# Kernel tuning notes

Hardware: AMD Instinct MI355X
Metric: run time of the kernel (lower is better)

## Reference

```python
import math
import jax, jax.numpy as jnp
import numpy as np
from jax import lax

D = 384; NHEAD = 12; NLAYERS = 4; H = 128; WIN = (128, 24); NS = (1, 10); B = 256; CONV_C = 128

def _interleave(s, c):
    # [s0,c0,s1,c1,...] along last dim (matches 0::2=sin, 1::2=cos)
    return jnp.stack([s, c], axis=-1).reshape(s.shape[:-1] + (s.shape[-1] * 2,))

def _pos_encoding():
    d3 = D // 3
    div = jnp.exp(jnp.arange(0, d3, 2, dtype=jnp.float32) * (-math.log(10000.0) / d3))
    coord = jnp.arange(H, dtype=jnp.float32) - H // 2
    pe1d = _interleave(jnp.sin(coord[:, None] * div), jnp.cos(coord[:, None] * div))  # (H, d3)
    pe_y = jnp.broadcast_to(pe1d[:, None, :], (H, H, d3))
    pe_x = jnp.broadcast_to(pe1d[None, :, :], (H, H, d3))
    ws = jnp.array(WIN, dtype=jnp.float32)
    pe_w = _interleave(jnp.sin(ws[:, None] * div), jnp.cos(ws[:, None] * div))  # (2, d3)
    pe_yx = jnp.concatenate([pe_y, pe_x], axis=-1)  # (H, H, 2*d3)
    pe = jnp.concatenate([
        jnp.broadcast_to(pe_yx[:, :, None, :], (H, H, len(WIN), 2 * d3)),
        jnp.broadcast_to(pe_w[None, None, :, :], (H, H, len(WIN), d3))], axis=-1)
    return pe  # (H, H, 2, D)

def _windows(img3, pos, ws):
    # img3: (B,3,H,W); pos: (n,2) int. Crop [y1:y2, x1:x2] then zero-pad bottom/right to ws x ws.
    hw = ws // 2
    y = jnp.clip(pos[:, 0], 0, H - 1); x = jnp.clip(pos[:, 1], 0, H - 1)
    y1 = jnp.maximum(0, y - hw); y2 = jnp.minimum(H, y + hw)
    x1 = jnp.maximum(0, x - hw); x2 = jnp.minimum(H, x + hw)
    r = jnp.arange(ws)
    rows = y1[:, None] + r; cols = x1[:, None] + r  # (n, ws)
    mask = (rows < y2[:, None])[:, :, None] & (cols < x2[:, None])[:, None, :]  # (n, ws, ws)
    win = img3[:, :, jnp.clip(rows, 0, H - 1)[:, :, None], jnp.clip(cols, 0, H - 1)[:, None, :]]  # (B,3,n,ws,ws)
    win = jnp.where(mask[None, None], win, 0.0)
    return jnp.transpose(win, (0, 2, 1, 3, 4))  # (B, n, 3, ws, ws)

def _layer_norm(x, g, b):
    m = x.mean(-1, keepdims=True)
    v = ((x - m) ** 2).mean(-1, keepdims=True)
    return (x - m) / jnp.sqrt(v + 1e-5) * g + b

def _encoder_layer(x, Wqkv, bqkv, Wo, bo, g1, b1, g2, b2, W1, bf1, W2, bf2):
    Bsz, S, _ = x.shape
    dh = D // NHEAD
    qkv = x @ Wqkv.T + bqkv
    q, k, v = jnp.split(qkv, 3, axis=-1)
    heads = lambda t: t.reshape(Bsz, S, NHEAD, dh).transpose(0, 2, 1, 3)
    q, k, v = heads(q), heads(k), heads(v)
    att = jax.nn.softmax(jnp.einsum('bhqd,bhkd->bhqk', q, k) / math.sqrt(dh), axis=-1)
    o = jnp.einsum('bhqk,bhkd->bhqd', att, v).transpose(0, 2, 1, 3).reshape(Bsz, S, D)
    x = _layer_norm(x + o @ Wo.T + bo, g1, b1)
    ff = jax.nn.relu(x @ W1.T + bf1) @ W2.T + bf2
    return _layer_norm(x + ff, g2, b2)

def _normalize(v):
    return v / jnp.maximum(jnp.linalg.norm(v, axis=1, keepdims=True), 1e-12)

def _forward(pos0, pos1, rgb_image, conv_w, conv_b, ext_w, ext_b, proj_w, proj_b,
             Wqkv, bqkv, Wo, bo, ln1g, ln1b, ln2g, ln2b, Wff1, bff1, Wff2, bff2,
             rw1, rb1, rw2, rb2, uw1, ub1, uw2, ub2):
    Bsz = rgb_image.shape[0]
    img3 = rgb_image[:, :3]
    win0 = _windows(img3, pos0, WIN[0]).reshape(Bsz * NS[0], 3, WIN[0], WIN[0])
    win1 = _windows(img3, pos1, WIN[1])  # (B, 10, 3, 24, 24)
    h = lax.conv_general_dilated(win0, conv_w, (4, 4), 'SAME')
    h = jax.nn.relu(h + conv_b[None, :, None, None])
    f0 = (h.mean((2, 3)) @ ext_w.T + ext_b).reshape(Bsz, NS[0], D)
    f1 = win1.reshape(Bsz, NS[1], -1) @ proj_w.T + proj_b  # (B,10,D)
    feats = jnp.concatenate([f0, f1], axis=1)  # (B, 11, D)
    pe = _pos_encoding()
    pp = jnp.concatenate([
        jnp.concatenate([pos0, jnp.zeros((NS[0], 1), pos0.dtype)], axis=1),
        jnp.concatenate([pos1, jnp.ones((NS[1], 1), pos1.dtype)], axis=1)], axis=0)  # (11, 3)
    pf = pe[pp[:, 0], pp[:, 1], pp[:, 2]]  # (11, D)
    x = feats + pf[None]
    for i in range(NLAYERS):
        x = _encoder_layer(x, Wqkv[i], bqkv[i], Wo[i], bo[i], ln1g[i], ln1b[i],
                           ln2g[i], ln2b[i], Wff1[i], bff1[i], Wff2[i], bff2[i])
    m = x.mean(axis=1)
    r = jax.nn.relu(m @ rw1.T + rb1) @ rw2.T + rb2
    r1, r2 = r[:, :3], r[:, 3:]
    r2 = r2 - jnp.sum(r1 * r2, axis=1, keepdims=True) * r1
    r3 = jnp.cross(r1, r2)
    R = jnp.concatenate([_normalize(r1), _normalize(r2), _normalize(r3)], axis=1)
    uv = jax.nn.sigmoid(jax.nn.relu(m @ uw1.T + ub1) @ uw2.T + ub2)
    return (uv, R)

def setup_inputs():
    key = jax.random.key(0)
    ks = iter(jax.random.split(key, 40))
    w = lambda *s: jax.random.normal(next(ks), s, jnp.float32) * 0.02
    return dict(
        rgb_image=jax.random.uniform(next(ks), (B, 4, H, H), jnp.float32),
        pos0=jax.random.randint(next(ks), (NS[0], 2), 0, H).astype(jnp.int32),
        pos1=jax.random.randint(next(ks), (NS[1], 2), 0, H).astype(jnp.int32),
        conv_w=w(CONV_C, 3, 7, 7), conv_b=jnp.zeros((CONV_C,), jnp.float32),
        ext_w=w(D, CONV_C), ext_b=jnp.zeros((D,), jnp.float32),
        proj_w=w(D, WIN[1] * WIN[1] * 3), proj_b=jnp.zeros((D,), jnp.float32),
        Wqkv=w(NLAYERS, 3 * D, D), bqkv=jnp.zeros((NLAYERS, 3 * D), jnp.float32),
        Wo=w(NLAYERS, D, D), bo=jnp.zeros((NLAYERS, D), jnp.float32),
        ln1g=jnp.ones((NLAYERS, D), jnp.float32), ln1b=jnp.zeros((NLAYERS, D), jnp.float32),
        ln2g=jnp.ones((NLAYERS, D), jnp.float32), ln2b=jnp.zeros((NLAYERS, D), jnp.float32),
        Wff1=w(NLAYERS, 2048, D), bff1=jnp.zeros((NLAYERS, 2048), jnp.float32),
        Wff2=w(NLAYERS, D, 2048), bff2=jnp.zeros((NLAYERS, D), jnp.float32),
        rw1=w(D, D), rb1=jnp.zeros((D,), jnp.float32),
        rw2=w(6, D), rb2=jnp.zeros((6,), jnp.float32),
        uw1=w(D, D), ub1=jnp.zeros((D,), jnp.float32),
        uw2=w(2, D), ub2=jnp.zeros((2,), jnp.float32),
    )

def reference(rgb_image, pos0, pos1, conv_w, conv_b, ext_w, ext_b, proj_w, proj_b,
              Wqkv, bqkv, Wo, bo, ln1g, ln1b, ln2g, ln2b, Wff1, bff1, Wff2, bff2,
              rw1, rb1, rw2, rb2, uw1, ub1, uw2, ub2):
    return _forward(pos0, pos1, rgb_image, conv_w, conv_b, ext_w, ext_b, proj_w, proj_b,
                    Wqkv, bqkv, Wo, bo, ln1g, ln1b, ln2g, ln2b, Wff1, bff1, Wff2, bff2,
                    rw1, rb1, rw2, rb2, uw1, ub1, uw2, ub2)
```

## Files before the change

kernel.cpp:

```cpp
#include <hip/hip_runtime.h>
#include <hip/hip_bf16.h>

#define B_ 256
#define S_ 11
#define D_ 384
#define NHEAD_ 12

typedef const float* bfp;
typedef __attribute__((ext_vector_type(8))) __bf16 bf16x8;
typedef __attribute__((ext_vector_type(4))) float f32x4;

__device__ __forceinline__ bf16x8 ld8_b64(const __bf16* p) {
    union { unsigned long long q[2]; bf16x8 v; } u;
    u.q[0] = *reinterpret_cast<const unsigned long long*>(p);
    u.q[1] = *reinterpret_cast<const unsigned long long*>(p + 4);
    return u.v;
}

__device__ __forceinline__ void gl16(const __bf16* g, __bf16* l) {
    __builtin_amdgcn_global_load_lds(
        (const __attribute__((address_space(1))) void*)g,
        (__attribute__((address_space(3))) void*)l, 16, 0, 0);
}

__global__ void prep_k(const float* __restrict__ proj_w, const float* __restrict__ Wqkv,
                       const float* __restrict__ Wo, const float* __restrict__ Wff1,
                       const float* __restrict__ Wff2,
                       __bf16* __restrict__ projWb, __bf16* __restrict__ WqkvB,
                       __bf16* __restrict__ WoB, __bf16* __restrict__ Wff1B,
                       __bf16* __restrict__ Wff2B,
                       const float* __restrict__ cw, __bf16* __restrict__ wpad,
                       const int* __restrict__ pos0, const int* __restrict__ pos1,
                       float* __restrict__ pf)
{
    int i = blockIdx.x * 256 + threadIdx.x;
    const float* s; __bf16* d; int off;
    if      (i < 165888)  { s = proj_w; d = projWb; off = i; }
    else if (i < 608256)  { s = Wqkv;   d = WqkvB;  off = i - 165888; }
    else if (i < 755712)  { s = Wo;     d = WoB;    off = i - 608256; }
    else if (i < 1542144) { s = Wff1;   d = Wff1B;  off = i - 755712; }
    else if (i < 2328576) { s = Wff2;   d = Wff2B;  off = i - 1542144; }
    else if (i < 2331648) {
        int e = i - 2328576;
        int r = e >> 5, g = e & 31;
        if (g >= 24) return;
        union { __bf16 h[8]; uint4 u; } w;
        #pragma unroll
        for (int kx = 0; kx < 8; ++kx) {
            float v = 0.f;
            if (g < 21 && kx < 7) v = cw[(size_t)r * 147 + g * 7 + kx];
            w.h[kx] = (__bf16)v;
        }
        *reinterpret_cast<uint4*>(&wpad[(size_t)r * 192 + g * 8]) = w.u;
        return;
    }
    else if (i < 2332032) {
        int dd0 = i - 2331648;
        const float c1 = -logf(10000.f) / 128.f;
        for (int ss = 0; ss < 11; ++ss) {
            int py, px, pw;
            if (ss == 0) { py = pos0[0]; px = pos0[1]; pw = 0; }
            else { py = pos1[(ss - 1) * 2]; px = pos1[(ss - 1) * 2 + 1]; pw = 1; }
            float coordv; int dd = dd0;
            if (dd0 < 128) coordv = (float)(py - 64);
            else if (dd0 < 256) { coordv = (float)(px - 64); dd = dd0 - 128; }
            else { coordv = (pw == 0) ? 128.f : 24.f; dd = dd0 - 256; }
            int ii = dd >> 1;
            float div = expf((float)(2 * ii) * c1);
            float ang = coordv * div;
            pf[ss * 384 + dd0] = (dd & 1) ? cosf(ang) : sinf(ang);
        }
        return;
    }
    else return;
    float4 v = reinterpret_cast<const float4*>(s)[off];
    union { __bf16 h[4]; unsigned long long u; } p;
    p.h[0] = (__bf16)v.x; p.h[1] = (__bf16)v.y;
    p.h[2] = (__bf16)v.z; p.h[3] = (__bf16)v.w;
    reinterpret_cast<unsigned long long*>(d)[off] = p.u;
}

__global__ __launch_bounds__(256) void gemm_bb_k(
    const __bf16* __restrict__ A, const __bf16* __restrict__ W,
    const float* __restrict__ bias, const float* __restrict__ resid,
    void* __restrict__ C_, int M, int N, int K, int mode, int outBf16, int kChunk)
{
    __shared__ __align__(16) __bf16 AsF[2][4096];
    __shared__ __align__(16) __bf16 WsF[2][4096];
    const int tid = threadIdx.x;
    const int bm = blockIdx.y * 64, bn = blockIdx.x * 64;
    const int z = blockIdx.z;
    int kStart = 0, kEnd = K;
    if (kChunk) { kStart = z * kChunk; kEnd = min(K, kStart + kChunk); }
    const int lane = tid & 63, wv = tid >> 6;
    const int wr = (wv >> 1) * 32, wc = (wv & 1) * 32;
    const int lr = lane & 15, lk = lane >> 4;
    const int c1 = tid + 256;
    const int r0 = tid >> 3, j0 = (tid & 7) ^ (r0 & 7);
    const int r1 = c1 >> 3,  j1 = (c1 & 7) ^ (r1 & 7);
    const size_t gaoff0 = (size_t)(bm + r0) * K + j0 * 8;
    const size_t gaoff1 = (size_t)(bm + r1) * K + j1 * 8;
    const size_t gwoff0 = (size_t)(bn + r0) * K + j0 * 8;
    const size_t gwoff1 = (size_t)(bn + r1) * K + j1 * 8;
    f32x4 acc[2][2] = {};

#define STAGE_(bf, kk) do {                                   \
        gl16(A + gaoff0 + (kk), &AsF[bf][(wv << 9)]);         \
        gl16(A + gaoff1 + (kk), &AsF[bf][2048 + (wv << 9)]);  \
        gl16(W + gwoff0 + (kk), &WsF[bf][(wv << 9)]);         \
        gl16(W + gwoff1 + (kk), &WsF[bf][2048 + (wv << 9)]);  \
    } while (0)

    STAGE_(0, kStart);
    __syncthreads();
    int cur = 0;
    for (int k0 = kStart; k0 < kEnd; k0 += 64) {
        if (k0 + 64 < kEnd) STAGE_(cur ^ 1, k0 + 64);
        const __bf16* Ab = AsF[cur];
        const __bf16* Wb = WsF[cur];
        #pragma unroll
        for (int s = 0; s < 2; ++s) {
            int j = s * 4 + lk;
            int ra0 = wr + lr,  ra1 = wr + 16 + lr;
            int rw0 = wc + lr,  rw1 = wc + 16 + lr;
            bf16x8 a0 = *reinterpret_cast<const bf16x8*>(&Ab[ra0 * 64 + ((j ^ (ra0 & 7)) << 3)]);
            bf16x8 a1 = *reinterpret_cast<const bf16x8*>(&Ab[ra1 * 64 + ((j ^ (ra1 & 7)) << 3)]);
            bf16x8 w0 = *reinterpret_cast<const bf16x8*>(&Wb[rw0 * 64 + ((j ^ (rw0 & 7)) << 3)]);
            bf16x8 w1 = *reinterpret_cast<const bf16x8*>(&Wb[rw1 * 64 + ((j ^ (rw1 & 7)) << 3)]);
            acc[0][0] = __builtin_amdgcn_mfma_f32_16x16x32_bf16(a0, w0, acc[0][0], 0, 0, 0);
            acc[0][1] = __builtin_amdgcn_mfma_f32_16x16x32_bf16(a0, w1, acc[0][1], 0, 0, 0);
            acc[1][0] = __builtin_amdgcn_mfma_f32_16x16x32_bf16(a1, w0, acc[1][0], 0, 0, 0);
            acc[1][1] = __builtin_amdgcn_mfma_f32_16x16x32_bf16(a1, w1, acc[1][1], 0, 0, 0);
        }
        __syncthreads();
        cur ^= 1;
    }
#undef STAGE_
    if (kChunk) {
        float* Cp = (float*)C_ + (size_t)z * M * N;
        #pragma unroll
        for (int m = 0; m < 2; ++m)
            #pragma unroll
            for (int n = 0; n < 2; ++n) {
                int col = bn + wc + n * 16 + lr;
                #pragma unroll
                for (int i = 0; i < 4; ++i) {
                    int row = bm + wr + m * 16 + lk * 4 + i;
                    Cp[(size_t)row * N + col] = acc[m][n][i];
                }
            }
    } else {
        #pragma unroll
        for (int m = 0; m < 2; ++m)
            #pragma unroll
            for (int n = 0; n < 2; ++n) {
                int col = bn + wc + n * 16 + lr;
                float bcol = bias[col];
                #pragma unroll
                for (int i = 0; i < 4; ++i) {
                    int row = bm + wr + m * 16 + lk * 4 + i;
                    float v = acc[m][n][i] + bcol;
                    if (mode == 1) v = fmaxf(v, 0.f);
                    if (mode == 2) v += resid[(size_t)row * N + col];
                    if (outBf16) ((__bf16*)C_)[(size_t)row * N + col] = (__bf16)v;
                    else         ((float*)C_)[(size_t)row * N + col] = v;
                }
            }
    }
}

__global__ __launch_bounds__(256) void convgemm_k(
    bfp __restrict__ img, const __bf16* __restrict__ wpad, bfp __restrict__ cb,
    const int* __restrict__ pos0, float* __restrict__ f0pre)
{
    __shared__ __align__(16) __bf16 Wlds[64][200];
    __shared__ __align__(16) __bf16 P[3][12][136];
    const int tid = threadIdx.x;
    const int blk = blockIdx.x;
    const int b = blk >> 3;
    const int bn = ((blk >> 2) & 1) * 64;
    const int mtg = blk & 3;
    int y = min(max(pos0[0], 0), 127), x = min(max(pos0[1], 0), 127);
    int y1 = max(0, y - 64), y2 = min(128, y + 64);
    int x1 = max(0, x - 64), x2 = min(128, x + 64);
    const int lane = tid & 63, wv = tid >> 6;
    const int wr = (wv >> 1) * 32, wc = (wv & 1) * 32;
    const int lr = lane & 15, lk = lane >> 4;
    const int oyl = wr >> 5;
    const int ox0 = lr, ox1 = 16 + lr;

    for (int e = tid; e < 1536; e += 256) {
        int r = e / 24, g = e - r * 24;
        uint4 q = *reinterpret_cast<const uint4*>(&wpad[(size_t)(bn + r) * 192 + g * 8]);
        *reinterpret_cast<uint4*>(&Wlds[r][g * 8]) = q;
    }

    float s0 = 0.f, s1 = 0.f;
    const float bc0 = cb[bn + wc + lr];
    const float bc1 = cb[bn + wc + 16 + lr];

    for (int t = 0; t < 4; ++t) {
        int mt = mtg * 4 + t;
        __syncthreads();
        for (int e = tid; e < 2448; e += 256) {
            int c = e / 816, rem = e - c * 816;
            int r2 = rem / 68, ip2 = (rem - r2 * 68) * 2;
            int rl = mt * 8 - 1 + r2;
            bool rok = (rl >= 0) && ((y1 + rl) < y2);
            const float* row = img + ((size_t)(b * 4 + c) * 128 + y1 + rl) * 128 + x1;
            int cl0 = ip2 - 1, cl1 = ip2;
            float v0 = 0.f, v1 = 0.f;
            if (rok && cl0 >= 0 && (x1 + cl0) < x2) v0 = row[cl0];
            if (rok && (x1 + cl1) < x2)             v1 = row[cl1];
            union { __bf16 h[2]; unsigned int u; } p;
            p.h[0] = (__bf16)v0; p.h[1] = (__bf16)v1;
            *reinterpret_cast<unsigned int*>(&P[c][r2][ip2]) = p.u;
        }
        __syncthreads();
        f32x4 acc[2][2] = {};
        #pragma unroll
        for (int kk = 0; kk < 6; ++kk) {
            int g = kk * 4 + lk;
            int c = g / 7, ky = g - c * 7;
            if (g >= 21) { c = 0; ky = 0; }
            const __bf16* prow = &P[c][oyl * 4 + ky][0];
            bf16x8 a0 = ld8_b64(prow + ox0 * 4);
            bf16x8 a1 = ld8_b64(prow + ox1 * 4);
            bf16x8 w0 = *reinterpret_cast<const bf16x8*>(&Wlds[wc + lr][g * 8]);
            bf16x8 w1 = *reinterpret_cast<const bf16x8*>(&Wlds[wc + 16 + lr][g * 8]);
            acc[0][0] = __builtin_amdgcn_mfma_f32_16x16x32_bf16(a0, w0, acc[0][0], 0, 0, 0);
            acc[0][1] = __builtin_amdgcn_mfma_f32_16x16x32_bf16(a0, w1, acc[0][1], 0, 0, 0);
            acc[1][0] = __builtin_amdgcn_mfma_f32_16x16x32_bf16(a1, w0, acc[1][0], 0, 0, 0);
            acc[1][1] = __builtin_amdgcn_mfma_f32_16x16x32_bf16(a1, w1, acc[1][1], 0, 0, 0);
        }
        #pragma unroll
        for (int m = 0; m < 2; ++m)
            #pragma unroll
            for (int i = 0; i < 4; ++i) {
                s0 += fmaxf(acc[m][0][i] + bc0, 0.f);
                s1 += fmaxf(acc[m][1][i] + bc1, 0.f);
            }
    }
    s0 += __shfl_xor(s0, 16); s0 += __shfl_xor(s0, 32);
    s1 += __shfl_xor(s1, 16); s1 += __shfl_xor(s1, 32);
    if (lk == 0) {
        atomicAdd(&f0pre[b * 128 + bn + wc + lr],      s0 * (1.f / 1024.f));
        atomicAdd(&f0pre[b * 128 + bn + wc + 16 + lr], s1 * (1.f / 1024.f));
    }
}

#define BM 64
#define BN 64
#define BK 16
__global__ __launch_bounds__(256) void gemm_k(
    const float* __restrict__ A, bfp __restrict__ W,
    bfp __restrict__ bias, const float* __restrict__ resid,
    float* __restrict__ C, int M, int N, int K, int mode)
{
    __shared__ __align__(16) float As[BK][BM + 4];
    __shared__ __align__(16) float Ws[BK][BN + 4];
    const int tx = threadIdx.x & 15, ty = threadIdx.x >> 4;
    const int bm = blockIdx.y * BM, bn = blockIdx.x * BN;
    float acc[4][4] = {};
    for (int k0 = 0; k0 < K; k0 += BK) {
        for (int e = threadIdx.x; e < BM * BK; e += 256) {
            int r = e >> 4, kk = e & 15;
            As[kk][r] = A[(size_t)(bm + r) * K + k0 + kk];
        }
        for (int e = threadIdx.x; e < BN * BK; e += 256) {
            int c = e >> 4, kk = e & 15;
            Ws[kk][c] = W[(size_t)(bn + c) * K + k0 + kk];
        }
        __syncthreads();
        #pragma unroll
        for (int kk = 0; kk < BK; ++kk) {
            float4 av = *reinterpret_cast<const float4*>(&As[kk][ty * 4]);
            float4 wv = *reinterpret_cast<const float4*>(&Ws[kk][tx * 4]);
            float a[4] = {av.x, av.y, av.z, av.w};
            float w[4] = {wv.x, wv.y, wv.z, wv.w};
            #pragma unroll
            for (int i = 0; i < 4; ++i)
                #pragma unroll
                for (int j = 0; j < 4; ++j) acc[i][j] += a[i] * w[j];
        }
        __syncthreads();
    }
    #pragma unroll
    for (int i = 0; i < 4; ++i) {
        int row = bm + ty * 4 + i;
        #pragma unroll
        for (int j = 0; j < 4; ++j) {
            int col = bn + tx * 4 + j;
            float v = acc[i][j] + bias[col];
            if (mode == 1) v = fmaxf(v, 0.f);
            if (mode == 2) v += resid[(size_t)row * N + col];
            C[(size_t)row * N + col] = v;
        }
    }
}

__global__ void f0_k(const float* __restrict__ f0pre, bfp __restrict__ ew,
                     bfp __restrict__ eb, float* __restrict__ fbuf0)
{
    int b = blockIdx.x, d = threadIdx.x;
    __shared__ float pre[128];
    if (d < 128) pre[d] = f0pre[b * 128 + d];
    __syncthreads();
    float acc = eb[d];
    for (int co = 0; co < 128; ++co) acc += pre[co] * ew[d * 128 + co];
    fbuf0[b * 384 + d] = acc;
}

__global__ void win1_k(bfp __restrict__ img, const int* __restrict__ pos1,
                       __bf16* __restrict__ w1)
{
    int i = blockIdx.x * 256 + threadIdx.x;
    if (i >= B_ * 10 * 1728) return;
    int cc = i % 24, r = (i / 24) % 24, c = (i / 576) % 3, s = (i / 1728) % 10, b = i / 17280;
    int y = min(max(pos1[s * 2], 0), 127), x = min(max(pos1[s * 2 + 1], 0), 127);
    int y1 = max(0, y - 12), y2 = min(128, y + 12);
    int x1 = max(0, x - 12), x2 = min(128, x + 12);
    float v = 0.f;
    if ((y1 + r) < y2 && (x1 + cc) < x2)
        v = img[((size_t)(b * 4 + c) * 128 + (y1 + r)) * 128 + (x1 + cc)];
    w1[i] = (__bf16)v;
}

__global__ void assemble_k(const float* __restrict__ f0, const float* __restrict__ p0,
                           const float* __restrict__ p1, const float* __restrict__ projb,
                           const float* __restrict__ pf, float* __restrict__ x,
                           __bf16* __restrict__ xb)
{
    int i = blockIdx.x * 256 + threadIdx.x;
    if (i >= B_ * S_ * D_) return;
    int d = i % 384, s = (i / 384) % 11, b = i / (384 * 11);
    float f;
    if (s == 0) f = f0[b * 384 + d];
    else {
        size_t o = ((size_t)(b * 10) + (s - 1)) * 384 + d;
        f = p0[o] + p1[o] + projb[d];
    }
    float v = f + pf[s * 384 + d];
    x[i] = v;
    xb[i] = (__bf16)v;
}

__global__ __launch_bounds__(128) void attn_k(const float* __restrict__ qkv,
                                              __bf16* __restrict__ obuf)
{
    int b = blockIdx.x / NHEAD_, h = blockIdx.x % NHEAD_;
    __shared__ float q[11][32], k[11][32], v[11][32], att[11][12];
    for (int e = threadIdx.x; e < 352; e += 128) {
        int s = e >> 5, d = e & 31;
        size_t base = (size_t)(b * 11 + s) * 1152 + h * 32 + d;
        q[s][d] = qkv[base];
        k[s][d] = qkv[base + 384];
        v[s][d] = qkv[base + 768];
    }
    __syncthreads();
    if (threadIdx.x < 121) {
        int i = threadIdx.x / 11, j = threadIdx.x % 11;
        float s = 0.f;
        #pragma unroll
        for (int d = 0; d < 32; ++d) s += q[i][d] * k[j][d];
        att[i][j] = s * 0.17677669529663687f;
    }
    __syncthreads();
    if (threadIdx.x < 11) {
        int i = threadIdx.x;
        float mx = att[i][0];
        for (int j = 1; j < 11; ++j) mx = fmaxf(mx, att[i][j]);
        float e_[11], sum = 0.f;
        for (int j = 0; j < 11; ++j) { e_[j] = expf(att[i][j] - mx); sum += e_[j]; }
        float inv = 1.f / sum;
        for (int j = 0; j < 11; ++j) att[i][j] = e_[j] * inv;
    }
    __syncthreads();
    for (int e = threadIdx.x; e < 352; e += 128) {
        int i = e >> 5, d = e & 31;
        float s = 0.f;
        #pragma unroll
        for (int j = 0; j < 11; ++j) s += att[i][j] * v[j][d];
        obuf[(size_t)(b * 11 + i) * 384 + h * 32 + d] = (__bf16)s;
    }
}

__global__ __launch_bounds__(512) void ln_k(const float* __restrict__ parts, int nparts,
                                            const float* __restrict__ resid,
                                            const float* __restrict__ bias,
                                            bfp g, bfp be, float* __restrict__ xo,
                                            __bf16* __restrict__ xb)
{
    int row = blockIdx.x * 8 + (threadIdx.x >> 6);
    int lane = threadIdx.x & 63;
    const size_t MN = (size_t)2816 * 384;
    float v[6];
    float s = 0.f, sq = 0.f;
    #pragma unroll
    for (int j = 0; j < 6; ++j) {
        int d = lane + 64 * j;
        size_t off = (size_t)row * 384 + d;
        float t = resid[off] + bias[d];
        for (int z = 0; z < nparts; ++z) t += parts[z * MN + off];
        v[j] = t; s += t; sq += t * t;
    }
    #pragma unroll
    for (int o = 32; o >= 1; o >>= 1) { s += __shfl_xor(s, o); sq += __shfl_xor(sq, o); }
    float mean = s * (1.f / 384.f);
    float var = sq * (1.f / 384.f) - mean * mean;
    float inv = rsqrtf(var + 1e-5f);
    float* xr = xo + (size_t)row * 384;
    __bf16* xbr = xb + (size_t)row * 384;
    #pragma unroll
    for (int j = 0; j < 6; ++j) {
        int d = lane + 64 * j;
        float o = (v[j] - mean) * inv * g[d] + be[d];
        xr[d] = o;
        xbr[d] = (__bf16)o;
    }
}

__global__ void mean_k(const float* __restrict__ x, float* __restrict__ m)
{
    int b = blockIdx.x, d = threadIdx.x;
    float s = 0.f;
    for (int si = 0; si < 11; ++si) s += x[((size_t)b * 11 + si) * 384 + d];
    m[b * 384 + d] = s * (1.f / 11.f);
}

__global__ __launch_bounds__(64) void head_k(const float* __restrict__ h1,
    const float* __restrict__ h2, bfp __restrict__ rw2, bfp __restrict__ rb2,
    bfp __restrict__ uw2, bfp __restrict__ ub2, float* __restrict__ out)
{
    int b = blockIdx.x, lane = threadIdx.x;
    float acc[8] = {};
    for (int d = lane; d < 384; d += 64) {
        float a1 = h1[b * 384 + d], a2 = h2[b * 384 + d];
        #pragma unroll
        for (int o = 0; o < 6; ++o) acc[o] += a1 * rw2[o * 384 + d];
        acc[6] += a2 * uw2[d];
        acc[7] += a2 * uw2[384 + d];
    }
    #pragma unroll
    for (int o = 0; o < 8; ++o)
        #pragma unroll
        for (int off = 32; off >= 1; off >>= 1) acc[o] += __shfl_xor(acc[o], off);
    if (lane == 0) {
        float r[6];
        for (int o = 0; o < 6; ++o) r[o] = acc[o] + rb2[o];
        float u0 = acc[6] + ub2[0], u1 = acc[7] + ub2[1];
        float dot12 = r[0] * r[3] + r[1] * r[4] + r[2] * r[5];
        float q2x = r[3] - dot12 * r[0], q2y = r[4] - dot12 * r[1], q2z = r[5] - dot12 * r[2];
        float q3x = r[1] * q2z - r[2] * q2y;
        float q3y = r[2] * q2x - r[0] * q2z;
        float q3z = r[0] * q2y - r[1] * q2x;
        float n1 = fmaxf(sqrtf(r[0]*r[0] + r[1]*r[1] + r[2]*r[2]), 1e-12f);
        float n2 = fmaxf(sqrtf(q2x*q2x + q2y*q2y + q2z*q2z), 1e-12f);
        float n3 = fmaxf(sqrtf(q3x*q3x + q3y*q3y + q3z*q3z), 1e-12f);
        out[b * 2 + 0] = 1.f / (1.f + expf(-u0));
        out[b * 2 + 1] = 1.f / (1.f + expf(-u1));
        float* R = out + B_ * 2 + b * 9;
        R[0] = r[0] / n1; R[1] = r[1] / n1; R[2] = r[2] / n1;
        R[3] = q2x / n2;  R[4] = q2y / n2;  R[5] = q2z / n2;
        R[6] = q3x / n3;  R[7] = q3y / n3;  R[8] = q3z / n3;
    }
}

extern "C" void kernel_launch(void* const* d_in, const int* in_sizes, int n_in,
                              void* d_out, int out_size, void* d_ws, size_t ws_size,
                              hipStream_t stream)
{
    bfp rgb     = (bfp)d_in[0];
    const int* pos0 = (const int*)d_in[1];
    const int* pos1 = (const int*)d_in[2];
    bfp conv_w  = (bfp)d_in[3];
    bfp conv_b  = (bfp)d_in[4];
    bfp ext_w   = (bfp)d_in[5];
    bfp ext_b   = (bfp)d_in[6];
    bfp proj_w  = (bfp)d_in[7];
    bfp proj_b  = (bfp)d_in[8];
    bfp Wqkv    = (bfp)d_in[9];
    bfp bqkv    = (bfp)d_in[10];
    bfp Wo      = (bfp)d_in[11];
    bfp bo      = (bfp)d_in[12];
    bfp ln1g    = (bfp)d_in[13];
    bfp ln1b    = (bfp)d_in[14];
    bfp ln2g    = (bfp)d_in[15];
    bfp ln2b    = (bfp)d_in[16];
    bfp Wff1    = (bfp)d_in[17];
    bfp bff1    = (bfp)d_in[18];
    bfp Wff2    = (bfp)d_in[19];
    bfp bff2    = (bfp)d_in[20];
    bfp rw1     = (bfp)d_in[21];
    bfp rb1     = (bfp)d_in[22];
    bfp rw2     = (bfp)d_in[23];
    bfp rb2     = (bfp)d_in[24];
    bfp uw1     = (bfp)d_in[25];
    bfp ub1     = (bfp)d_in[26];
    bfp uw2     = (bfp)d_in[27];
    bfp ub2     = (bfp)d_in[28];

    float* ws = (float*)d_ws;
    float*  X      = ws;
    float*  QKV    = ws + 2162688;
    float*  FBUF0  = QKV + 983040;
    float*  F0PRE  = QKV + 983040 + 98304;
    float*  PP0    = QKV + 1114112;
    float*  PP1    = QKV + 1114112 + 983040;
    __bf16* OBUFb  = (__bf16*)(ws + 5406720);
    float*  H1     = ws + 5947392;
    float*  H2     = ws + 6045696;
    __bf16* FFH16  = (__bf16*)(ws + 6144000);
    __bf16* WIN1F16= FFH16;
    float*  PF     = ws + 9027584;
    float*  M_     = ws + 9031808;
    __bf16* Xb     = (__bf16*)(ws + 9130112);
    __bf16* projWb = (__bf16*)(ws + 9670784);
    __bf16* WqkvB  = (__bf16*)(ws + 10002560);
    __bf16* WoB    = (__bf16*)(ws + 10887296);
    __bf16* Wff1B  = (__bf16*)(ws + 11182208);
    __bf16* Wff2B  = (__bf16*)(ws + 12755072);
    __bf16* WpadC  = (__bf16*)(ws + 14327936);

    hipMemsetAsync(F0PRE, 0, 256 * 128 * sizeof(float), stream);

    prep_k<<<9110, 256, 0, stream>>>(proj_w, Wqkv, Wo, Wff1, Wff2,
                                     projWb, WqkvB, WoB, Wff1B, Wff2B,
                                     conv_w, WpadC, pos0, pos1, PF);

    convgemm_k<<<2048, 256, 0, stream>>>(rgb, WpadC, conv_b, pos0, F0PRE);
    win1_k<<<(B_ * 10 * 1728 + 255) / 256, 256, 0, stream>>>(rgb, pos1, WIN1F16);
    f0_k<<<256, 384, 0, stream>>>(F0PRE, ext_w, ext_b, FBUF0);
    gemm_bb_k<<<dim3(6, 40, 2), 256, 0, stream>>>(WIN1F16, projWb, nullptr, nullptr,
                                                  PP0, 2560, 384, 1728, 0, 0, 896);
    assemble_k<<<(B_ * S_ * D_ + 255) / 256, 256, 0, stream>>>(FBUF0, PP0, PP1, proj_b,
                                                               PF, X, Xb);

    for (int i = 0; i < 4; ++i) {
        gemm_bb_k<<<dim3(18, 44), 256, 0, stream>>>(
            Xb, WqkvB + (size_t)i * 1152 * 384, bqkv + i * 1152, nullptr, QKV,
            2816, 1152, 384, 0, 0, 0);
        attn_k<<<B_ * NHEAD_, 128, 0, stream>>>(QKV, OBUFb);
        gemm_bb_k<<<dim3(6, 44, 2), 256, 0, stream>>>(
            OBUFb, WoB + (size_t)i * 384 * 384, nullptr, nullptr, QKV,
            2816, 384, 384, 0, 0, 192);
        ln_k<<<352, 512, 0, stream>>>(QKV, 2, X, bo + i * 384,
                                      ln1g + i * 384, ln1b + i * 384, X, Xb);
        gemm_bb_k<<<dim3(32, 44), 256, 0, stream>>>(
            Xb, Wff1B + (size_t)i * 2048 * 384, bff1 + i * 2048, nullptr, FFH16,
            2816, 2048, 384, 1, 1, 0);
        gemm_bb_k<<<dim3(6, 44, 3), 256, 0, stream>>>(
            FFH16, Wff2B + (size_t)i * 384 * 2048, nullptr, nullptr, QKV,
            2816, 384, 2048, 0, 0, 704);
        ln_k<<<352, 512, 0, stream>>>(QKV, 3, X, bff2 + i * 384,
                                      ln2g + i * 384, ln2b + i * 384, X, Xb);
    }

    mean_k<<<256, 384, 0, stream>>>(X, M_);
    gemm_k<<<dim3(384 / BN, 256 / BM), 256, 0, stream>>>(M_, rw1, rb1, nullptr, H1, 256, 384, 384, 1);
    gemm_k<<<dim3(384 / BN, 256 / BM), 256, 0, stream>>>(M_, uw1, ub1, nullptr, H2, 256, 384, 384, 1);
    head_k<<<256, 64, 0, stream>>>(H1, H2, rw2, rb2, uw2, ub2, (float*)d_out);
}
```

Before: 520.5 us.

## Enlarge bf16 GEMM M-tile to 128, fuse f0 into assemble and head kernels

The bf16 MFMA GEMM now uses 128x64 output tiles, with each wave computing 64x32, so every loaded W fragment is reused across four A fragments and the grid height halves. The f0 projection is folded into assemble_k, and mean, the two hidden GEMMs and the head are merged into one per-batch kernel, which removes several launches and intermediate buffers. The cost is more LDS and accumulator registers per block, and fewer blocks for the smaller GEMMs, which may leave CUs underoccupied. The s==0 path in assemble now recomputes a 128-length dot product per element.

Measured after the change: 488.9 us. 6.1% less time.

```diff
diff --git a/kernel.cpp b/kernel.cpp
--- a/kernel.cpp
+++ b/kernel.cpp
@@ -85,30 +85,36 @@
     const float* __restrict__ bias, const float* __restrict__ resid,
     void* __restrict__ C_, int M, int N, int K, int mode, int outBf16, int kChunk)
 {
-    __shared__ __align__(16) __bf16 AsF[2][4096];
+    __shared__ __align__(16) __bf16 AsF[2][8192];
     __shared__ __align__(16) __bf16 WsF[2][4096];
     const int tid = threadIdx.x;
-    const int bm = blockIdx.y * 64, bn = blockIdx.x * 64;
+    const int bm = blockIdx.y * 128, bn = blockIdx.x * 64;
     const int z = blockIdx.z;
     int kStart = 0, kEnd = K;
     if (kChunk) { kStart = z * kChunk; kEnd = min(K, kStart + kChunk); }
     const int lane = tid & 63, wv = tid >> 6;
-    const int wr = (wv >> 1) * 32, wc = (wv & 1) * 32;
+    const int wrA = (wv >> 1) * 64, wcW = (wv & 1) * 32;
     const int lr = lane & 15, lk = lane >> 4;
-    const int c1 = tid + 256;
-    const int r0 = tid >> 3, j0 = (tid & 7) ^ (r0 & 7);
-    const int r1 = c1 >> 3,  j1 = (c1 & 7) ^ (r1 & 7);
-    const size_t gaoff0 = (size_t)(bm + r0) * K + j0 * 8;
-    const size_t gaoff1 = (size_t)(bm + r1) * K + j1 * 8;
-    const size_t gwoff0 = (size_t)(bn + r0) * K + j0 * 8;
-    const size_t gwoff1 = (size_t)(bn + r1) * K + j1 * 8;
-    f32x4 acc[2][2] = {};
-
-#define STAGE_(bf, kk) do {                                   \
-        gl16(A + gaoff0 + (kk), &AsF[bf][(wv << 9)]);         \
-        gl16(A + gaoff1 + (kk), &AsF[bf][2048 + (wv << 9)]);  \
-        gl16(W + gwoff0 + (kk), &WsF[bf][(wv << 9)]);         \
-        gl16(W + gwoff1 + (kk), &WsF[bf][2048 + (wv << 9)]);  \
+    size_t gaoff[4], gwoff[2];
+    #pragma unroll
+    for (int k = 0; k < 4; ++k) {
+        int c = tid + k * 256; int r = c >> 3; int j = (c & 7) ^ (r & 7);
+        gaoff[k] = (size_t)(bm + r) * K + j * 8;
+    }
+    #pragma unroll
+    for (int k = 0; k < 2; ++k) {
+        int c = tid + k * 256; int r = c >> 3; int j = (c & 7) ^ (r & 7);
+        gwoff[k] = (size_t)(bn + r) * K + j * 8;
+    }
+    f32x4 acc[4][2] = {};
+
+#define STAGE_(bf, kk) do {                                       \
+        gl16(A + gaoff[0] + (kk), &AsF[bf][(wv << 9)]);           \
+        gl16(A + gaoff[1] + (kk), &AsF[bf][2048 + (wv << 9)]);    \
+        gl16(A + gaoff[2] + (kk), &AsF[bf][4096 + (wv << 9)]);    \
+        gl16(A + gaoff[3] + (kk), &AsF[bf][6144 + (wv << 9)]);    \
+        gl16(W + gwoff[0] + (kk), &WsF[bf][(wv << 9)]);           \
+        gl16(W + gwoff[1] + (kk), &WsF[bf][2048 + (wv << 9)]);    \
     } while (0)
 
     STAGE_(0, kStart);
@@ -121,16 +127,16 @@
         #pragma unroll
         for (int s = 0; s < 2; ++s) {
             int j = s * 4 + lk;
-            int ra0 = wr + lr,  ra1 = wr + 16 + lr;
-            int rw0 = wc + lr,  rw1 = wc + 16 + lr;
-            bf16x8 a0 = *reinterpret_cast<const bf16x8*>(&Ab[ra0 * 64 + ((j ^ (ra0 & 7)) << 3)]);
-            bf16x8 a1 = *reinterpret_cast<const bf16x8*>(&Ab[ra1 * 64 + ((j ^ (ra1 & 7)) << 3)]);
+            int rw0 = wcW + lr, rw1_ = wcW + 16 + lr;
             bf16x8 w0 = *reinterpret_cast<const bf16x8*>(&Wb[rw0 * 64 + ((j ^ (rw0 & 7)) << 3)]);
-            bf16x8 w1 = *reinterpret_cast<const bf16x8*>(&Wb[rw1 * 64 + ((j ^ (rw1 & 7)) << 3)]);
-            acc[0][0] = __builtin_amdgcn_mfma_f32_16x16x32_bf16(a0, w0, acc[0][0], 0, 0, 0);
-            acc[0][1] = __builtin_amdgcn_mfma_f32_16x16x32_bf16(a0, w1, acc[0][1], 0, 0, 0);
-            acc[1][0] = __builtin_amdgcn_mfma_f32_16x16x32_bf16(a1, w0, acc[1][0], 0, 0, 0);
-            acc[1][1] = __builtin_amdgcn_mfma_f32_16x16x32_bf16(a1, w1, acc[1][1], 0, 0, 0);
+            bf16x8 w1 = *reinterpret_cast<const bf16x8*>(&Wb[rw1_ * 64 + ((j ^ (rw1_ & 7)) << 3)]);
+            #pragma unroll
+            for (int m = 0; m < 4; ++m) {
+                int ra = wrA + m * 16 + lr;
+                bf16x8 a = *reinterpret_cast<const bf16x8*>(&Ab[ra * 64 + ((j ^ (ra & 7)) << 3)]);
+                acc[m][0] = __builtin_amdgcn_mfma_f32_16x16x32_bf16(a, w0, acc[m][0], 0, 0, 0);
+                acc[m][1] = __builtin_amdgcn_mfma_f32_16x16x32_bf16(a, w1, acc[m][1], 0, 0, 0);
+            }
         }
         __syncthreads();
         cur ^= 1;
@@ -139,26 +145,26 @@
     if (kChunk) {
         float* Cp = (float*)C_ + (size_t)z * M * N;
         #pragma unroll
-        for (int m = 0; m < 2; ++m)
+        for (int m = 0; m < 4; ++m)
             #pragma unroll
             for (int n = 0; n < 2; ++n) {
-                int col = bn + wc + n * 16 + lr;
+                int col = bn + wcW + n * 16 + lr;
                 #pragma unroll
                 for (int i = 0; i < 4; ++i) {
-                    int row = bm + wr + m * 16 + lk * 4 + i;
+                    int row = bm + wrA + m * 16 + lk * 4 + i;
                     Cp[(size_t)row * N + col] = acc[m][n][i];
                 }
             }
     } else {
         #pragma unroll
-        for (int m = 0; m < 2; ++m)
+        for (int m = 0; m < 4; ++m)
             #pragma unroll
             for (int n = 0; n < 2; ++n) {
-                int col = bn + wc + n * 16 + lr;
+                int col = bn + wcW + n * 16 + lr;
                 float bcol = bias[col];
                 #pragma unroll
                 for (int i = 0; i < 4; ++i) {
-                    int row = bm + wr + m * 16 + lk * 4 + i;
+                    int row = bm + wrA + m * 16 + lk * 4 + i;
                     float v = acc[m][n][i] + bcol;
                     if (mode == 1) v = fmaxf(v, 0.f);
                     if (mode == 2) v += resid[(size_t)row * N + col];
@@ -249,68 +255,6 @@
     }
 }
 
-#define BM 64
-#define BN 64
-#define BK 16
-__global__ __launch_bounds__(256) void gemm_k(
-    const float* __restrict__ A, bfp __restrict__ W,
-    bfp __restrict__ bias, const float* __restrict__ resid,
-    float* __restrict__ C, int M, int N, int K, int mode)
-{
-    __shared__ __align__(16) float As[BK][BM + 4];
-    __shared__ __align__(16) float Ws[BK][BN + 4];
-    const int tx = threadIdx.x & 15, ty = threadIdx.x >> 4;
-    const int bm = blockIdx.y * BM, bn = blockIdx.x * BN;
-    float acc[4][4] = {};
-    for (int k0 = 0; k0 < K; k0 += BK) {
-        for (int e = threadIdx.x; e < BM * BK; e += 256) {
-            int r = e >> 4, kk = e & 15;
-            As[kk][r] = A[(size_t)(bm + r) * K + k0 + kk];
-        }
-        for (int e = threadIdx.x; e < BN * BK; e += 256) {
-            int c = e >> 4, kk = e & 15;
-            Ws[kk][c] = W[(size_t)(bn + c) * K + k0 + kk];
-        }
-        __syncthreads();
-        #pragma unroll
-        for (int kk = 0; kk < BK; ++kk) {
-            float4 av = *reinterpret_cast<const float4*>(&As[kk][ty * 4]);
-            float4 wv = *reinterpret_cast<const float4*>(&Ws[kk][tx * 4]);
-            float a[4] = {av.x, av.y, av.z, av.w};
-            float w[4] = {wv.x, wv.y, wv.z, wv.w};
-            #pragma unroll
-            for (int i = 0; i < 4; ++i)
-                #pragma unroll
-                for (int j = 0; j < 4; ++j) acc[i][j] += a[i] * w[j];
-        }
-        __syncthreads();
-    }
-    #pragma unroll
-    for (int i = 0; i < 4; ++i) {
-        int row = bm + ty * 4 + i;
-        #pragma unroll
-        for (int j = 0; j < 4; ++j) {
-            int col = bn + tx * 4 + j;
-            float v = acc[i][j] + bias[col];
-            if (mode == 1) v = fmaxf(v, 0.f);
-            if (mode == 2) v += resid[(size_t)row * N + col];
-            C[(size_t)row * N + col] = v;
-        }
-    }
-}
-
-__global__ void f0_k(const float* __restrict__ f0pre, bfp __restrict__ ew,
-                     bfp __restrict__ eb, float* __restrict__ fbuf0)
-{
-    int b = blockIdx.x, d = threadIdx.x;
-    __shared__ float pre[128];
-    if (d < 128) pre[d] = f0pre[b * 128 + d];
-    __syncthreads();
-    float acc = eb[d];
-    for (int co = 0; co < 128; ++co) acc += pre[co] * ew[d * 128 + co];
-    fbuf0[b * 384 + d] = acc;
-}
-
 __global__ void win1_k(bfp __restrict__ img, const int* __restrict__ pos1,
                        __bf16* __restrict__ w1)
 {
@@ -326,8 +270,10 @@
     w1[i] = (__bf16)v;
 }
 
-__global__ void assemble_k(const float* __restrict__ f0, const float* __restrict__ p0,
-                           const float* __restrict__ p1, const float* __restrict__ projb,
+__global__ void assemble_k(const float* __restrict__ f0pre, bfp __restrict__ ew,
+                           bfp __restrict__ eb,
+                           const float* __restrict__ p0, const float* __restrict__ p1,
+                           const float* __restrict__ projb,
                            const float* __restrict__ pf, float* __restrict__ x,
                            __bf16* __restrict__ xb)
 {
@@ -335,8 +281,14 @@
     if (i >= B_ * S_ * D_) return;
     int d = i % 384, s = (i / 384) % 11, b = i / (384 * 11);
     float f;
-    if (s == 0) f = f0[b * 384 + d];
-    else {
+    if (s == 0) {
+        float acc = eb[d];
+        const float* pre = f0pre + b * 128;
+        const float* wrow = ew + (size_t)d * 128;
+        #pragma unroll 4
+        for (int co = 0; co < 128; ++co) acc += pre[co] * wrow[co];
+        f = acc;
+    } else {
         size_t o = ((size_t)(b * 10) + (s - 1)) * 384 + d;
         f = p0[o] + p1[o] + projb[d];
     }
@@ -420,49 +372,63 @@
     }
 }
 
-__global__ void mean_k(const float* __restrict__ x, float* __restrict__ m)
-{
+__global__ __launch_bounds__(384) void headfused_k(
+    const float* __restrict__ X,
+    bfp __restrict__ rw1, bfp __restrict__ rb1, bfp __restrict__ uw1, bfp __restrict__ ub1,
+    bfp __restrict__ rw2, bfp __restrict__ rb2, bfp __restrict__ uw2, bfp __restrict__ ub2,
+    float* __restrict__ out)
+{
+    __shared__ float m[384], h1s[384], h2s[384];
     int b = blockIdx.x, d = threadIdx.x;
     float s = 0.f;
-    for (int si = 0; si < 11; ++si) s += x[((size_t)b * 11 + si) * 384 + d];
-    m[b * 384 + d] = s * (1.f / 11.f);
-}
-
-__global__ __launch_bounds__(64) void head_k(const float* __restrict__ h1,
-    const float* __restrict__ h2, bfp __restrict__ rw2, bfp __restrict__ rb2,
-    bfp __restrict__ uw2, bfp __restrict__ ub2, float* __restrict__ out)
-{
-    int b = blockIdx.x, lane = threadIdx.x;
-    float acc[8] = {};
-    for (int d = lane; d < 384; d += 64) {
-        float a1 = h1[b * 384 + d], a2 = h2[b * 384 + d];
-        #pragma unroll
-        for (int o = 0; o < 6; ++o) acc[o] += a1 * rw2[o * 384 + d];
-        acc[6] += a2 * uw2[d];
-        acc[7] += a2 * uw2[384 + d];
-    }
-    #pragma unroll
-    for (int o = 0; o < 8; ++o)
-        #pragma unroll
-        for (int off = 32; off >= 1; off >>= 1) acc[o] += __shfl_xor(acc[o], off);
-    if (lane == 0) {
-        float r[6];
-        for (int o = 0; o < 6; ++o) r[o] = acc[o] + rb2[o];
-        float u0 = acc[6] + ub2[0], u1 = acc[7] + ub2[1];
-        float dot12 = r[0] * r[3] + r[1] * r[4] + r[2] * r[5];
-        float q2x = r[3] - dot12 * r[0], q2y = r[4] - dot12 * r[1], q2z = r[5] - dot12 * r[2];
-        float q3x = r[1] * q2z - r[2] * q2y;
-        float q3y = r[2] * q2x - r[0] * q2z;
-        float q3z = r[0] * q2y - r[1] * q2x;
-        float n1 = fmaxf(sqrtf(r[0]*r[0] + r[1]*r[1] + r[2]*r[2]), 1e-12f);
-        float n2 = fmaxf(sqrtf(q2x*q2x + q2y*q2y + q2z*q2z), 1e-12f);
-        float n3 = fmaxf(sqrtf(q3x*q3x + q3y*q3y + q3z*q3z), 1e-12f);
-        out[b * 2 + 0] = 1.f / (1.f + expf(-u0));
-        out[b * 2 + 1] = 1.f / (1.f + expf(-u1));
-        float* R = out + B_ * 2 + b * 9;
-        R[0] = r[0] / n1; R[1] = r[1] / n1; R[2] = r[2] / n1;
-        R[3] = q2x / n2;  R[4] = q2y / n2;  R[5] = q2z / n2;
-        R[6] = q3x / n3;  R[7] = q3y / n3;  R[8] = q3z / n3;
+    for (int si = 0; si < 11; ++si) s += X[((size_t)b * 11 + si) * 384 + d];
+    m[d] = s * (1.f / 11.f);
+    __syncthreads();
+    float a1 = rb1[d], a2 = ub1[d];
+    const float4* r4 = reinterpret_cast<const float4*>(rw1 + (size_t)d * 384);
+    const float4* u4 = reinterpret_cast<const float4*>(uw1 + (size_t)d * 384);
+    for (int k4 = 0; k4 < 96; ++k4) {
+        float4 wv1 = r4[k4], wv2 = u4[k4];
+        const float* mk = &m[k4 * 4];
+        a1 += mk[0] * wv1.x + mk[1] * wv1.y + mk[2] * wv1.z + mk[3] * wv1.w;
+        a2 += mk[0] * wv2.x + mk[1] * wv2.y + mk[2] * wv2.z + mk[3] * wv2.w;
+    }
+    h1s[d] = fmaxf(a1, 0.f);
+    h2s[d] = fmaxf(a2, 0.f);
+    __syncthreads();
+    if (d < 64) {
+        int lane = d;
+        float acc[8] = {};
+        for (int dd = lane; dd < 384; dd += 64) {
+            float v1 = h1s[dd], v2 = h2s[dd];
+            #pragma unroll
+            for (int o = 0; o < 6; ++o) acc[o] += v1 * rw2[o * 384 + dd];
+            acc[6] += v2 * uw2[dd];
+            acc[7] += v2 * uw2[384 + dd];
+        }
+        #pragma unroll
+        for (int o = 0; o < 8; ++o)
+            #pragma unroll
+            for (int off = 32; off >= 1; off >>= 1) acc[o] += __shfl_xor(acc[o], off);
+        if (lane == 0) {
+            float r[6];
+            for (int o = 0; o < 6; ++o) r[o] = acc[o] + rb2[o];
+            float u0 = acc[6] + ub2[0], u1 = acc[7] + ub2[1];
+            float dot12 = r[0] * r[3] + r[1] * r[4] + r[2] * r[5];
+            float q2x = r[3] - dot12 * r[0], q2y = r[4] - dot12 * r[1], q2z = r[5] - dot12 * r[2];
+            float q3x = r[1] * q2z - r[2] * q2y;
+            float q3y = r[2] * q2x - r[0] * q2z;
+            float q3z = r[0] * q2y - r[1] * q2x;
+            float n1 = fmaxf(sqrtf(r[0]*r[0] + r[1]*r[1] + r[2]*r[2]), 1e-12f);
+            float n2 = fmaxf(sqrtf(q2x*q2x + q2y*q2y + q2z*q2z), 1e-12f);
+            float n3 = fmaxf(sqrtf(q3x*q3x + q3y*q3y + q3z*q3z), 1e-12f);
+            out[b * 2 + 0] = 1.f / (1.f + expf(-u0));
+            out[b * 2 + 1] = 1.f / (1.f + expf(-u1));
+            float* R = out + B_ * 2 + b * 9;
+            R[0] = r[0] / n1; R[1] = r[1] / n1; R[2] = r[2] / n1;
+            R[3] = q2x / n2;  R[4] = q2y / n2;  R[5] = q2z / n2;
+            R[6] = q3x / n3;  R[7] = q3y / n3;  R[8] = q3z / n3;
+        }
     }
 }
 
@@ -503,17 +469,13 @@
     float* ws = (float*)d_ws;
     float*  X      = ws;
     float*  QKV    = ws + 2162688;
-    float*  FBUF0  = QKV + 983040;
-    float*  F0PRE  = QKV + 983040 + 98304;
+    float*  F0PRE  = QKV + 1081344;
     float*  PP0    = QKV + 1114112;
     float*  PP1    = QKV + 1114112 + 983040;
     __bf16* OBUFb  = (__bf16*)(ws + 5406720);
-    float*  H1     = ws + 5947392;
-    float*  H2     = ws + 6045696;
     __bf16* FFH16  = (__bf16*)(ws + 6144000);
     __bf16* WIN1F16= FFH16;
     float*  PF     = ws + 9027584;
-    float*  M_     = ws + 9031808;
     __bf16* Xb     = (__bf16*)(ws + 9130112);
     __bf16* projWb = (__bf16*)(ws + 9670784);
     __bf16* WqkvB  = (__bf16*)(ws + 10002560);
@@ -530,34 +492,31 @@
 
     convgemm_k<<<2048, 256, 0, stream>>>(rgb, WpadC, conv_b, pos0, F0PRE);
     win1_k<<<(B_ * 10 * 1728 + 255) / 256, 256, 0, stream>>>(rgb, pos1, WIN1F16);
-    f0_k<<<256, 384, 0, stream>>>(F0PRE, ext_w, ext_b, FBUF0);
-    gemm_bb_k<<<dim3(6, 40, 2), 256, 0, stream>>>(WIN1F16, projWb, nullptr, nullptr,
+    gemm_bb_k<<<dim3(6, 20, 2), 256, 0, stream>>>(WIN1F16, projWb, nullptr, nullptr,
                                                   PP0, 2560, 384, 1728, 0, 0, 896);
-    assemble_k<<<(B_ * S_ * D_ + 255) / 256, 256, 0, stream>>>(FBUF0, PP0, PP1, proj_b,
-                                                               PF, X, Xb);
+    assemble_k<<<(B_ * S_ * D_ + 255) / 256, 256, 0, stream>>>(
+        F0PRE, ext_w, ext_b, PP0, PP1, proj_b, PF, X, Xb);
 
     for (int i = 0; i < 4; ++i) {
-        gemm_bb_k<<<dim3(18, 44), 256, 0, stream>>>(
+        gemm_bb_k<<<dim3(18, 22), 256, 0, stream>>>(
             Xb, WqkvB + (size_t)i * 1152 * 384, bqkv + i * 1152, nullptr, QKV,
             2816, 1152, 384, 0, 0, 0);
         attn_k<<<B_ * NHEAD_, 128, 0, stream>>>(QKV, OBUFb);
-        gemm_bb_k<<<dim3(6, 44, 2), 256, 0, stream>>>(
+        gemm_bb_k<<<dim3(6, 22, 2), 256, 0, stream>>>(
             OBUFb, WoB + (size_t)i * 384 * 384, nullptr, nullptr, QKV,
             2816, 384, 384, 0, 0, 192);
         ln_k<<<352, 512, 0, stream>>>(QKV, 2, X, bo + i * 384,
                                       ln1g + i * 384, ln1b + i * 384, X, Xb);
-        gemm_bb_k<<<dim3(32, 44), 256, 0, stream>>>(
+        gemm_bb_k<<<dim3(32, 22), 256, 0, stream>>>(
             Xb, Wff1B + (size_t)i * 2048 * 384, bff1 + i * 2048, nullptr, FFH16,
             2816, 2048, 384, 1, 1, 0);
-        gemm_bb_k<<<dim3(6, 44, 3), 256, 0, stream>>>(
+        gemm_bb_k<<<dim3(6, 22, 3), 256, 0, stream>>>(
             FFH16, Wff2B + (size_t)i * 384 * 2048, nullptr, nullptr, QKV,
             2816, 384, 2048, 0, 0, 704);
         ln_k<<<352, 512, 0, stream>>>(QKV, 3, X, bff2 + i * 384,
                                       ln2g + i * 384, ln2b + i * 384, X, Xb);
     }
 
-    mean_k<<<256, 384, 0, stream>>>(X, M_);
-    gemm_k<<<dim3(384 / BN, 256 / BM), 256, 0, stream>>>(M_, rw1, rb1, nullptr, H1, 256, 384, 384, 1);
-    gemm_k<<<dim3(384 / BN, 256 / BM), 256, 0, stream>>>(M_, uw1, ub1, nullptr, H2, 256, 384, 384, 1);
-    head_k<<<256, 64, 0, stream>>>(H1, H2, rw2, rb2, uw2, ub2, (float*)d_out);
-}
+    headfused_k<<<256, 384, 0, stream>>>(X, rw1, rb1, uw1, ub1,
+                                         rw2, rb2, uw2, ub2, (float*)d_out);
+}
```
